# Kernel optimization log

Hardware: AMD Instinct MI355X
Metric: run time of the kernel (lower is better)

The kernel has to match this reference:

```python
import jax, jax.numpy as jnp
import numpy as np
from jax import lax

DN = ('NCHW', 'OIHW', 'NCHW')


def _conv(x, w, pad):
    return lax.conv_general_dilated(x, w, (1, 1), [(pad, pad), (pad, pad)], dimension_numbers=DN)


def _bn(x, gamma, beta, mean, var, eps=1e-5):
    inv = gamma * lax.rsqrt(var + eps)
    return x * inv[None, :, None, None] + (beta - mean * inv)[None, :, None, None]


def _unfold(x, K, pad):
    # torch.nn.Unfold layout: channel-major, kernel positions fastest -> (B, C, K*K, H, W)
    B, C, H, W = x.shape
    p = lax.conv_general_dilated_patches(x, (K, K), (1, 1), [(pad, pad), (pad, pad)], dimension_numbers=DN)
    return p.reshape(B, C, K * K, H, W)


def setup_inputs() -> dict:
    key = jax.random.key(0)
    ks = jax.random.split(key, 16)
    B, C, H, W, K = 16, 64, 64, 64, 3
    d = {
        'x': jax.random.normal(ks[0], (B, C, H, W), jnp.float32),
        'wq': jax.random.normal(ks[1], (C, C, 1, 1), jnp.float32) * 0.1,
        'wk': jax.random.normal(ks[2], (C, C, K, K), jnp.float32) * 0.05,
        'wv': jax.random.normal(ks[3], (C, C, 1, 1), jnp.float32) * 0.1,
        'pos_h': jax.random.normal(ks[4], (C, K, 1), jnp.float32),
        'pos_w': jax.random.normal(ks[5], (C, 1, K), jnp.float32),
    }
    for i, nm in enumerate(['q', 'k', 'v', 'o']):
        d[nm + '_gamma'] = jnp.ones((C,), jnp.float32)
        d[nm + '_beta'] = jnp.zeros((C,), jnp.float32)
        d[nm + '_mean'] = jax.random.normal(ks[6 + i], (C,), jnp.float32) * 0.1
        d[nm + '_var'] = jax.random.uniform(ks[10 + i], (C,), jnp.float32, 0.5, 1.5)
    return d


def reference(x, wq, q_gamma, q_beta, q_mean, q_var,
              wk, k_gamma, k_beta, k_mean, k_var,
              wv, v_gamma, v_beta, v_mean, v_var,
              pos_h, pos_w, o_gamma, o_beta, o_mean, o_var):
    B, C, H, W = x.shape
    K = pos_h.shape[1]
    heads = C // 8
    cph = C // heads  # channels per head

    q = jax.nn.relu(_bn(_conv(x, wq, 0), q_gamma, q_beta, q_mean, q_var))
    k = jax.nn.relu(_bn(_conv(x, wk, K // 2), k_gamma, k_beta, k_mean, k_var))
    v = _bn(_conv(x, wv, 0), v_gamma, v_beta, v_mean, v_var)

    # local keys + positional bias: (B, C, K*K, H, W)
    unfold_k = _unfold(k, K, K // 2)
    pos = (pos_h + pos_w).reshape(1, C, K * K, 1, 1)
    kp = (unfold_k + pos).reshape(B, heads, cph, K * K, H, W)
    qh = q.reshape(B, heads, cph, 1, H, W)

    attn = (qh * kp).sum(axis=2)            # (B, heads, K*K, H, W)
    attn = jax.nn.softmax(attn, axis=2)

    # local aggregation (LocalConvolution): weights shared across cph channels per head
    uv = _unfold(v, K, (K - 1) // 2).reshape(B, heads, cph, K * K, H, W)
    out = (attn[:, :, None] * uv).sum(axis=3).reshape(B, C, H, W)

    out = jax.nn.relu(_bn(out, o_gamma, o_beta, o_mean, o_var))
    return out
```

## Files before the change

kernel.cpp:

```cpp
#include <hip/hip_runtime.h>
#include <hip/hip_bf16.h>
#include <math.h>

#define B_ 16
#define C_ 64
#define H_ 64
#define W_ 64
#define KSTEPS 18

typedef __attribute__((ext_vector_type(8))) short bf16x8;
typedef __attribute__((ext_vector_type(4))) short bf16x4;
typedef __attribute__((ext_vector_type(4))) float f32x4;

static __device__ __forceinline__ unsigned short f2b(float f) {
    __hip_bfloat16 h = __float2bfloat16(f);
    return *reinterpret_cast<unsigned short*>(&h);
}
static __device__ __forceinline__ float b2f(unsigned short u) {
    __hip_bfloat16 h;
    *reinterpret_cast<unsigned short*>(&h) = u;
    return __bfloat162float(h);
}

__global__ __launch_bounds__(64) void prep_kernel(
    const float* __restrict__ wq, const float* __restrict__ wk, const float* __restrict__ wv,
    const float* __restrict__ qg, const float* __restrict__ qb, const float* __restrict__ qm, const float* __restrict__ qv,
    const float* __restrict__ kg, const float* __restrict__ kb, const float* __restrict__ km, const float* __restrict__ kv,
    const float* __restrict__ vg, const float* __restrict__ vb, const float* __restrict__ vm, const float* __restrict__ vv,
    const float* __restrict__ og, const float* __restrict__ ob, const float* __restrict__ om, const float* __restrict__ ov,
    unsigned short* __restrict__ Wp, float* __restrict__ bnp)
{
    const int bid = blockIdx.x;
    const int lane = threadIdx.x;
    if (bid < 12 * KSTEPS) {
        const int mf = bid / KSTEPS;
        const int ks = bid % KSTEPS;
        const int r = lane & 15;
        bf16x8 u;
#pragma unroll
        for (int j = 0; j < 8; j++) {
            int k = ks * 32 + ((lane >> 4) << 3) + j;
            int tap = k >> 6;
            int c = k & 63;
            float w;
            if (mf < 4)      { int co = mf * 16 + r;        w = (tap == 4) ? wq[co * 64 + c] : 0.f; }
            else if (mf < 8) { int co = (mf - 4) * 16 + r;  w = wk[(co * 64 + c) * 9 + tap]; }
            else             { int co = (mf - 8) * 16 + r;  w = (tap == 4) ? wv[co * 64 + c] : 0.f; }
            u[j] = (short)f2b(w);
        }
        *reinterpret_cast<bf16x8*>(Wp + ((size_t)(mf * KSTEPS + ks) * 64 + lane) * 8) = u;
    } else {
        const int c = lane;
        const float* G[4] = {qg, kg, vg, og};
        const float* Bt[4] = {qb, kb, vb, ob};
        const float* M[4] = {qm, km, vm, om};
        const float* V[4] = {qv, kv, vv, ov};
#pragma unroll
        for (int p = 0; p < 4; p++) {
            float inv = G[p][c] * rsqrtf(V[p][c] + 1e-5f);
            bnp[p * 128 + c] = inv;
            bnp[p * 128 + 64 + c] = Bt[p][c] - M[p][c] * inv;
        }
    }
}

__global__ __launch_bounds__(256) void xt_kernel(
    const float* __restrict__ x, unsigned short* __restrict__ xt)
{
    __shared__ float ls[64][65];
    const int b = blockIdx.x >> 6;
    const int h = blockIdx.x & 63;
    const int tid = threadIdx.x;
    const int w = tid & 63;
    const int cg = tid >> 6;
#pragma unroll
    for (int cc = 0; cc < 16; cc++) {
        int c = cg * 16 + cc;
        ls[c][w] = x[((b * 64 + c) * 64 + h) * 64 + w];
    }
    __syncthreads();
    const int px = tid & 63;
    bf16x8 u0, u1;
#pragma unroll
    for (int j = 0; j < 8; j++) {
        u0[j] = (short)f2b(ls[cg * 16 + j][px]);
        u1[j] = (short)f2b(ls[cg * 16 + 8 + j][px]);
    }
    size_t base = ((size_t)((b * 64 + h) * 64 + px)) * 64 + cg * 16;
    *reinterpret_cast<bf16x8*>(xt + base) = u0;
    *reinterpret_cast<bf16x8*>(xt + base + 8) = u1;
}

#define KSM_OFF 0
#define VSM_OFF 25344
#define QSM_OFF 50688
__global__ __launch_bounds__(512, 4) void fused_kernel(
    const unsigned short* __restrict__ xt, const unsigned short* __restrict__ Wp,
    const float* __restrict__ bnp,
    const float* __restrict__ ph, const float* __restrict__ pw,
    float* __restrict__ out)
{
    __shared__ __align__(16) char smem[58880];
    __shared__ float bns[512];
    const int bid = blockIdx.x;
    const int b = bid >> 6;
    const int h = bid & 63;
    const int tid = threadIdx.x;

    for (int i = tid; i < 5 * 66 * 8; i += 512) {
        int ch  = i & 7;
        int col = (i >> 3) % 66;
        int dy  = (i >> 3) / 66;
        int gh = h - 2 + dy, gw = col - 1;
        bf16x8 u = (bf16x8){0,0,0,0,0,0,0,0};
        if ((unsigned)gh < 64u && (unsigned)gw < 64u)
            u = *reinterpret_cast<const bf16x8*>(xt + ((size_t)((b * 64 + gh) * 64 + gw)) * 64 + ch * 8);
        int La = ((dy * 66 + col) * 64 + ch * 8) * 2;
        La ^= (col & 7) << 4;
        *reinterpret_cast<bf16x8*>(smem + La) = u;
    }
    bns[tid < 512 ? tid : 0] = bnp[tid < 512 ? tid : 0];
    __syncthreads();

    const int wid = tid >> 6, lane = tid & 63;
    const int mfg = wid >> 1, nfg = wid & 1;
    const int t = lane & 15, q4 = lane >> 4;

    f32x4 acc[3][6];
#pragma unroll
    for (int m = 0; m < 3; m++)
#pragma unroll
        for (int n = 0; n < 6; n++) acc[m][n] = (f32x4){0.f, 0.f, 0.f, 0.f};

    for (int ks = 0; ks < KSTEPS; ks++) {
        const int tap = ks >> 1;
        const int dy = tap / 3, dx = tap - dy * 3;
        const int kb = (ks & 1) * 32 + q4 * 8;
        bf16x8 bf[6];
#pragma unroll
        for (int n = 0; n < 6; n++) {
            int p = (nfg * 6 + n) * 16 + t;
            int r = p >> 6, colw = p & 63;
            int col = colw + dx;
            int La = (((r + dy) * 66 + col) * 64 + kb) * 2;
            La ^= (col & 7) << 4;
            bf[n] = *reinterpret_cast<const bf16x8*>(smem + La);
        }
#pragma unroll
        for (int m = 0; m < 3; m++) {
            int mf = mfg * 3 + m;
            bf16x8 af = *reinterpret_cast<const bf16x8*>(Wp + ((size_t)(mf * KSTEPS + ks) * 64 + lane) * 8);
#pragma unroll
            for (int n = 0; n < 6; n++)
                acc[m][n] = __builtin_amdgcn_mfma_f32_16x16x32_bf16(af, bf[n], acc[m][n], 0, 0, 0);
        }
    }
    __syncthreads();

#pragma unroll
    for (int m = 0; m < 3; m++) {
        int mf = mfg * 3 + m;
        int plane = mf >> 2;
        int c0 = (mf * 16 + q4 * 4) & 63;
        f32x4 inv  = *reinterpret_cast<const f32x4*>(&bns[plane * 128 + c0]);
        f32x4 bias = *reinterpret_cast<const f32x4*>(&bns[plane * 128 + 64 + c0]);
#pragma unroll
        for (int n = 0; n < 6; n++) {
            int p = (nfg * 6 + n) * 16 + t;
            int r = p >> 6, colw = p & 63;
            bf16x4 pack;
#pragma unroll
            for (int j = 0; j < 4; j++) {
                float val = acc[m][n][j] * inv[j] + bias[j];
                if (plane < 2) val = fmaxf(val, 0.f);
                pack[j] = (short)f2b(val);
            }
            if (plane == 0) {
                if (r == 1) {
                    int La = (colw * 64 + c0) * 2;
                    La ^= (colw & 7) << 4;
                    *reinterpret_cast<bf16x4*>(smem + QSM_OFF + La) = pack;
                }
            } else {
                int pxp = colw + 1;
                int La = ((r * 66 + pxp) * 64 + c0) * 2;
                La ^= (pxp & 7) << 4;
                *reinterpret_cast<bf16x4*>(smem + (plane == 1 ? KSM_OFF : VSM_OFF) + La) = pack;
            }
        }
    }
    __syncthreads();

    const bf16x8 z8 = (bf16x8){0,0,0,0,0,0,0,0};
    for (int i = tid; i < 96; i += 512) {
        int buf = i & 1;
        int j = i >> 1;
        int ch = j & 7;
        int jj = j >> 3;
        int col = (jj & 1) ? 65 : 0;
        int rr = jj >> 1;
        int La = ((rr * 66 + col) * 64 + ch * 8) * 2;
        La ^= (col & 7) << 4;
        *reinterpret_cast<bf16x8*>(smem + (buf ? VSM_OFF : KSM_OFF) + La) = z8;
    }
    int rbad = (h == 0) ? 0 : ((h == 63) ? 2 : -1);
    if (rbad >= 0) {
        for (int i = tid; i < 66 * 8 * 2; i += 512) {
            int buf = i & 1;
            int j = i >> 1;
            int ch = j & 7;
            int col = j >> 3;
            int La = ((rbad * 66 + col) * 64 + ch * 8) * 2;
            La ^= (col & 7) << 4;
            *reinterpret_cast<bf16x8*>(smem + (buf ? VSM_OFF : KSM_OFF) + La) = z8;
        }
    }
    __syncthreads();

    const int px = tid & 63;
    const int head = tid >> 6;
    const int cb = head * 8;

    float qf[8];
    {
        int Lq = (px * 64 + cb) * 2;
        Lq ^= (px & 7) << 4;
        bf16x8 q8 = *reinterpret_cast<const bf16x8*>(smem + QSM_OFF + Lq);
#pragma unroll
        for (int j = 0; j < 8; j++) qf[j] = b2f((unsigned short)q8[j]);
    }

    float A[3], Bx[3];
#pragma unroll
    for (int tt = 0; tt < 3; tt++) {
        float a = 0.f, bb = 0.f;
#pragma unroll
        for (int j = 0; j < 8; j++) {
            a  = fmaf(qf[j], ph[(cb + j) * 3 + tt], a);
            bb = fmaf(qf[j], pw[(cb + j) * 3 + tt], bb);
        }
        A[tt] = a; Bx[tt] = bb;
    }

    float logit[9];
#pragma unroll
    for (int dy = 0; dy < 3; dy++) {
#pragma unroll
        for (int dx = 0; dx < 3; dx++) {
            int pxp = px + dx;
            int La = ((dy * 66 + pxp) * 64 + cb) * 2;
            La ^= (pxp & 7) << 4;
            bf16x8 k8 = *reinterpret_cast<const bf16x8*>(smem + KSM_OFF + La);
            float qk = 0.f;
#pragma unroll
            for (int j = 0; j < 8; j++) qk = fmaf(qf[j], b2f((unsigned short)k8[j]), qk);
            logit[dy * 3 + dx] = qk + A[dy] + Bx[dx];
        }
    }

    float mx = logit[0];
#pragma unroll
    for (int tt = 1; tt < 9; tt++) mx = fmaxf(mx, logit[tt]);
    float e[9], sum = 0.f;
#pragma unroll
    for (int tt = 0; tt < 9; tt++) { e[tt] = __expf(logit[tt] - mx); sum += e[tt]; }
    float inv = 1.f / sum;

    float o[8];
#pragma unroll
    for (int j = 0; j < 8; j++) o[j] = 0.f;
#pragma unroll
    for (int dy = 0; dy < 3; dy++) {
#pragma unroll
        for (int dx = 0; dx < 3; dx++) {
            int pxp = px + dx;
            int La = ((dy * 66 + pxp) * 64 + cb) * 2;
            La ^= (pxp & 7) << 4;
            bf16x8 v8 = *reinterpret_cast<const bf16x8*>(smem + VSM_OFF + La);
            float w = e[dy * 3 + dx];
#pragma unroll
            for (int j = 0; j < 8; j++) o[j] = fmaf(w, b2f((unsigned short)v8[j]), o[j]);
        }
    }

#pragma unroll
    for (int j = 0; j < 8; j++) {
        int c = cb + j;
        float val = fmaxf(fmaf(o[j] * inv, bns[384 + c], bns[384 + 64 + c]), 0.f);
        out[((size_t)(b * C_ + c) * H_ + h) * W_ + px] = val;
    }
}

extern "C" void kernel_launch(void* const* d_in, const int* in_sizes, int n_in,
                              void* d_out, int out_size, void* d_ws, size_t ws_size,
                              hipStream_t stream)
{
    const float* x   = (const float*)d_in[0];
    const float* wq  = (const float*)d_in[1];
    const float* wk  = (const float*)d_in[2];
    const float* wv  = (const float*)d_in[3];
    const float* ph  = (const float*)d_in[4];
    const float* pw  = (const float*)d_in[5];
    const float* qg  = (const float*)d_in[6];
    const float* qb  = (const float*)d_in[7];
    const float* qm  = (const float*)d_in[8];
    const float* qv  = (const float*)d_in[9];
    const float* kg  = (const float*)d_in[10];
    const float* kb  = (const float*)d_in[11];
    const float* km  = (const float*)d_in[12];
    const float* kv  = (const float*)d_in[13];
    const float* vg  = (const float*)d_in[14];
    const float* vb  = (const float*)d_in[15];
    const float* vm  = (const float*)d_in[16];
    const float* vv  = (const float*)d_in[17];
    const float* og  = (const float*)d_in[18];
    const float* ob  = (const float*)d_in[19];
    const float* om  = (const float*)d_in[20];
    const float* ov  = (const float*)d_in[21];

    char* ws = (char*)d_ws;
    unsigned short* Wp = (unsigned short*)ws;
    float* bnp = (float*)(ws + 221184);
    unsigned short* xt = (unsigned short*)(ws + 223232);

    prep_kernel<<<12 * KSTEPS + 1, 64, 0, stream>>>(
        wq, wk, wv, qg, qb, qm, qv, kg, kb, km, kv, vg, vb, vm, vv,
        og, ob, om, ov, Wp, bnp);

    xt_kernel<<<B_ * H_, 256, 0, stream>>>(x, xt);

    fused_kernel<<<B_ * H_, 512, 0, stream>>>(xt, Wp, bnp, ph, pw, (float*)d_out);
}
```

Before: 157.3 us.

## Skip zero-weight MFMAs for 1x1 q/v convs and cache positional weights in LDS

The fused GEMM previously ran all 18 K-steps for the q, k and v planes even though q and v are 1x1 convolutions whose packed weights are zero outside the center tap. Now each wave owns one 16-channel slice. It runs the full k-conv, adds the v and q MFMAs only on the center-tap K-steps, and computes q only for the middle-row pixels it actually needs. The positional bias tables move into shared memory, and launch bounds relax to 2 blocks per SM so the larger accumulator set has more registers. The full unroll and lower occupancy hint could increase register pressure or reduce latency hiding.

New measurement: 180.3 us. 14.6% more time.

```diff
diff --git a/kernel.cpp b/kernel.cpp
--- a/kernel.cpp
+++ b/kernel.cpp
@@ -94,7 +94,7 @@
 #define KSM_OFF 0
 #define VSM_OFF 25344
 #define QSM_OFF 50688
-__global__ __launch_bounds__(512, 4) void fused_kernel(
+__global__ __launch_bounds__(512, 2) void fused_kernel(
     const unsigned short* __restrict__ xt, const unsigned short* __restrict__ Wp,
     const float* __restrict__ bnp,
     const float* __restrict__ ph, const float* __restrict__ pw,
@@ -102,6 +102,7 @@
 {
     __shared__ __align__(16) char smem[58880];
     __shared__ float bns[512];
+    __shared__ float phs[192], pws[192];
     const int bid = blockIdx.x;
     const int b = bid >> 6;
     const int h = bid & 63;
@@ -119,19 +120,21 @@
         La ^= (col & 7) << 4;
         *reinterpret_cast<bf16x8*>(smem + La) = u;
     }
-    bns[tid < 512 ? tid : 0] = bnp[tid < 512 ? tid : 0];
+    bns[tid & 511] = bnp[tid & 511];
+    if (tid < 192) { phs[tid] = ph[tid]; pws[tid] = pw[tid]; }
     __syncthreads();
 
     const int wid = tid >> 6, lane = tid & 63;
-    const int mfg = wid >> 1, nfg = wid & 1;
+    const int mf = wid & 3, half = wid >> 2;
     const int t = lane & 15, q4 = lane >> 4;
-
-    f32x4 acc[3][6];
-#pragma unroll
-    for (int m = 0; m < 3; m++)
-#pragma unroll
-        for (int n = 0; n < 6; n++) acc[m][n] = (f32x4){0.f, 0.f, 0.f, 0.f};
-
+    const int qbase = half ? 0 : 4;
+
+    f32x4 acck[6], accv[6], accq[2];
+#pragma unroll
+    for (int n = 0; n < 6; n++) { acck[n] = (f32x4){0.f,0.f,0.f,0.f}; accv[n] = (f32x4){0.f,0.f,0.f,0.f}; }
+    accq[0] = (f32x4){0.f,0.f,0.f,0.f}; accq[1] = (f32x4){0.f,0.f,0.f,0.f};
+
+#pragma unroll
     for (int ks = 0; ks < KSTEPS; ks++) {
         const int tap = ks >> 1;
         const int dy = tap / 3, dx = tap - dy * 3;
@@ -139,54 +142,64 @@
         bf16x8 bf[6];
 #pragma unroll
         for (int n = 0; n < 6; n++) {
-            int p = (nfg * 6 + n) * 16 + t;
+            int p = (half * 6 + n) * 16 + t;
             int r = p >> 6, colw = p & 63;
             int col = colw + dx;
             int La = (((r + dy) * 66 + col) * 64 + kb) * 2;
             La ^= (col & 7) << 4;
             bf[n] = *reinterpret_cast<const bf16x8*>(smem + La);
         }
-#pragma unroll
-        for (int m = 0; m < 3; m++) {
-            int mf = mfg * 3 + m;
-            bf16x8 af = *reinterpret_cast<const bf16x8*>(Wp + ((size_t)(mf * KSTEPS + ks) * 64 + lane) * 8);
+        bf16x8 afk = *reinterpret_cast<const bf16x8*>(Wp + ((size_t)((4 + mf) * KSTEPS + ks) * 64 + lane) * 8);
+#pragma unroll
+        for (int n = 0; n < 6; n++)
+            acck[n] = __builtin_amdgcn_mfma_f32_16x16x32_bf16(afk, bf[n], acck[n], 0, 0, 0);
+        if (ks == 8 || ks == 9) {
+            bf16x8 afq = *reinterpret_cast<const bf16x8*>(Wp + ((size_t)(mf * KSTEPS + ks) * 64 + lane) * 8);
+            bf16x8 afv = *reinterpret_cast<const bf16x8*>(Wp + ((size_t)((8 + mf) * KSTEPS + ks) * 64 + lane) * 8);
 #pragma unroll
             for (int n = 0; n < 6; n++)
-                acc[m][n] = __builtin_amdgcn_mfma_f32_16x16x32_bf16(af, bf[n], acc[m][n], 0, 0, 0);
-        }
-    }
-    __syncthreads();
-
-#pragma unroll
-    for (int m = 0; m < 3; m++) {
-        int mf = mfg * 3 + m;
-        int plane = mf >> 2;
-        int c0 = (mf * 16 + q4 * 4) & 63;
-        f32x4 inv  = *reinterpret_cast<const f32x4*>(&bns[plane * 128 + c0]);
-        f32x4 bias = *reinterpret_cast<const f32x4*>(&bns[plane * 128 + 64 + c0]);
+                accv[n] = __builtin_amdgcn_mfma_f32_16x16x32_bf16(afv, bf[n], accv[n], 0, 0, 0);
+            accq[0] = __builtin_amdgcn_mfma_f32_16x16x32_bf16(afq, bf[qbase], accq[0], 0, 0, 0);
+            accq[1] = __builtin_amdgcn_mfma_f32_16x16x32_bf16(afq, bf[qbase + 1], accq[1], 0, 0, 0);
+        }
+    }
+    __syncthreads();
+
+    const int c0 = mf * 16 + q4 * 4;
+    {
+        f32x4 invk  = *reinterpret_cast<const f32x4*>(&bns[128 + c0]);
+        f32x4 biask = *reinterpret_cast<const f32x4*>(&bns[128 + 64 + c0]);
+        f32x4 invv  = *reinterpret_cast<const f32x4*>(&bns[256 + c0]);
+        f32x4 biasv = *reinterpret_cast<const f32x4*>(&bns[256 + 64 + c0]);
 #pragma unroll
         for (int n = 0; n < 6; n++) {
-            int p = (nfg * 6 + n) * 16 + t;
+            int p = (half * 6 + n) * 16 + t;
             int r = p >> 6, colw = p & 63;
-            bf16x4 pack;
+            int pxp = colw + 1;
+            int La = ((r * 66 + pxp) * 64 + c0) * 2;
+            La ^= (pxp & 7) << 4;
+            bf16x4 pk, pv;
 #pragma unroll
             for (int j = 0; j < 4; j++) {
-                float val = acc[m][n][j] * inv[j] + bias[j];
-                if (plane < 2) val = fmaxf(val, 0.f);
-                pack[j] = (short)f2b(val);
+                pk[j] = (short)f2b(fmaxf(acck[n][j] * invk[j] + biask[j], 0.f));
+                pv[j] = (short)f2b(accv[n][j] * invv[j] + biasv[j]);
             }
-            if (plane == 0) {
-                if (r == 1) {
-                    int La = (colw * 64 + c0) * 2;
-                    La ^= (colw & 7) << 4;
-                    *reinterpret_cast<bf16x4*>(smem + QSM_OFF + La) = pack;
-                }
-            } else {
-                int pxp = colw + 1;
-                int La = ((r * 66 + pxp) * 64 + c0) * 2;
-                La ^= (pxp & 7) << 4;
-                *reinterpret_cast<bf16x4*>(smem + (plane == 1 ? KSM_OFF : VSM_OFF) + La) = pack;
-            }
+            *reinterpret_cast<bf16x4*>(smem + KSM_OFF + La) = pk;
+            *reinterpret_cast<bf16x4*>(smem + VSM_OFF + La) = pv;
+        }
+        f32x4 invq  = *reinterpret_cast<const f32x4*>(&bns[c0]);
+        f32x4 biasq = *reinterpret_cast<const f32x4*>(&bns[64 + c0]);
+#pragma unroll
+        for (int i = 0; i < 2; i++) {
+            int nq = 4 + half * 2 + i;
+            int colw = (nq & 3) * 16 + t;
+            int La = (colw * 64 + c0) * 2;
+            La ^= (colw & 7) << 4;
+            bf16x4 pq;
+#pragma unroll
+            for (int j = 0; j < 4; j++)
+                pq[j] = (short)f2b(fmaxf(accq[i][j] * invq[j] + biasq[j], 0.f));
+            *reinterpret_cast<bf16x4*>(smem + QSM_OFF + La) = pq;
         }
     }
     __syncthreads();
@@ -236,8 +249,8 @@
         float a = 0.f, bb = 0.f;
 #pragma unroll
         for (int j = 0; j < 8; j++) {
-            a  = fmaf(qf[j], ph[(cb + j) * 3 + tt], a);
-            bb = fmaf(qf[j], pw[(cb + j) * 3 + tt], bb);
+            a  = fmaf(qf[j], phs[(cb + j) * 3 + tt], a);
+            bb = fmaf(qf[j], pws[(cb + j) * 3 + tt], bb);
         }
         A[tt] = a; Bx[tt] = bb;
     }
```
